# Kernel tuning notes

Hardware: AMD Instinct MI355X
Metric: run time of the kernel (lower is better)

Reference implementation:

```python
import jax, jax.numpy as jnp
import numpy as np
from jax import lax

ALPHA = 2.0
EROSIONS = 10


def setup_inputs() -> dict:
    key = jax.random.key(0)
    k1, k2 = jax.random.split(key)
    B, C, H, W = 32, 1, 1024, 1024
    pred = jax.random.uniform(k1, (B, C, H, W), dtype=jnp.float32)
    target = jax.random.uniform(k2, (B, C, H, W), dtype=jnp.float32)
    return {"pred": pred, "target": target}


def _hausdorff_er_loss(pred, target):
    # 3x3 cross structuring element * 0.2 (sums to 1), as in kernel2D
    kernel = jnp.array([[0.0, 0.2, 0.0],
                        [0.2, 0.2, 0.2],
                        [0.0, 0.2, 0.0]], dtype=pred.dtype)
    kernel = kernel[None, None]  # OIHW: (1,1,3,3)

    bound = (pred - target) ** 2  # (B,1,H,W)

    def step(carry, k):
        b, acc = carry
        # scipy.ndimage.convolve(mode='constant', cval=0) == SAME zero-padded conv;
        # the cross kernel is symmetric so correlation == convolution.
        dil = lax.conv_general_dilated(
            b, kernel, window_strides=(1, 1), padding='SAME',
            dimension_numbers=('NCHW', 'OIHW', 'NCHW'))
        er = jnp.maximum(dil - 0.5, 0.0)
        # per-sample min/max normalization (ptp over the whole (1,H,W) array)
        emin = er.min(axis=(1, 2, 3), keepdims=True)
        emax = er.max(axis=(1, 2, 3), keepdims=True)
        ptp = emax - emin
        er = jnp.where(ptp > 0, (er - emin) / jnp.where(ptp > 0, ptp, 1.0), er)
        acc = acc + er * (k + 1.0) ** ALPHA
        return (er, acc), None

    ks = jnp.arange(EROSIONS, dtype=bound.dtype)
    (_, eroted), _ = lax.scan(step, (bound, jnp.zeros_like(bound)), ks)
    return eroted.mean()


def reference(pred, target):
    return _hausdorff_er_loss(pred, target)
```

## Files before the change

### kernel.cpp

```cpp
#include <hip/hip_runtime.h>

#define BATCH 32
#define HH 1024
#define WW 1024
#define NPIX (HH * WW)
#define NEROS 10
#define TPS 64
#define NTILES (BATCH * TPS)
#define NB0 (BATCH * 128)
#define FRPS 1024

__device__ __forceinline__ float4 ld4f(const float* p) {
    return *reinterpret_cast<const float4*>(p);
}


__global__ __launch_bounds__(512, 8) void conv0_kernel(
    const float* __restrict__ pred, const float* __restrict__ tgt,
    float* __restrict__ out, unsigned short* __restrict__ Fout,
    unsigned* __restrict__ cntOut, unsigned* __restrict__ omin,
    unsigned* __restrict__ omax, double* __restrict__ osum) {
    int blk = blockIdx.x;
    blk = (blk & 7) * (NB0 >> 3) + (blk >> 3);
    const int s = blk >> 7, ty = blk & 127, ry = ty << 3;
    const int tid = threadIdx.x, lane = tid & 63, w = tid >> 6;
    const size_t sbase = (size_t)s * NPIX;

    __shared__ float sb[10 * 1024];

    float4 pv[5], tv[5];
#pragma unroll
    for (int i = 0; i < 5; ++i) {
        const int slot = tid + 512 * i;
        const int y = ry - 1 + (slot >> 8);
        if (y >= 0 && y < HH) {
            const size_t idx = sbase + (size_t)y * WW + ((slot & 255) << 2);
            pv[i] = ld4f(pred + idx);
            tv[i] = ld4f(tgt + idx);
        } else {
            pv[i] = make_float4(0.f, 0.f, 0.f, 0.f);
            tv[i] = make_float4(0.f, 0.f, 0.f, 0.f);
        }
    }
#pragma unroll
    for (int i = 0; i < 5; ++i) {
        const int slot = tid + 512 * i;
        float4 b;
        b.x = (pv[i].x - tv[i].x) * (pv[i].x - tv[i].x);
        b.y = (pv[i].y - tv[i].y) * (pv[i].y - tv[i].y);
        b.z = (pv[i].z - tv[i].z) * (pv[i].z - tv[i].z);
        b.w = (pv[i].w - tv[i].w) * (pv[i].w - tv[i].w);
        *reinterpret_cast<float4*>(
            &sb[(slot >> 8) * 1024 + ((slot & 255) << 2)]) = b;
    }
    __syncthreads();

    float lmin = 3.4e38f, lmax = 0.f, lsum = 0.f;
    unsigned rowmask = 0u;
    const int y = ry + w;
#pragma unroll
    for (int q = 0; q < 4; ++q) {
        const int xw = (q << 8) + (lane << 2);
        const float4 U = *(const float4*)&sb[w * 1024 + xw];
        const float4 Cc = *(const float4*)&sb[(w + 1) * 1024 + xw];
        const float4 D = *(const float4*)&sb[(w + 2) * 1024 + xw];
        float lf = __shfl_up(Cc.w, 1);
        if (lane == 0) lf = (q > 0) ? sb[(w + 1) * 1024 + (q << 8) - 1] : 0.f;
        float rt = __shfl_down(Cc.x, 1);
        if (lane == 63)
            rt = (q < 3) ? sb[(w + 1) * 1024 + (q << 8) + 256] : 0.f;
        const float cv[4] = {Cc.x, Cc.y, Cc.z, Cc.w};
        const float uv[4] = {U.x, U.y, U.z, U.w};
        const float dv[4] = {D.x, D.y, D.z, D.w};
        const float lvv[4] = {lf, Cc.x, Cc.y, Cc.z};
        const float rvv[4] = {Cc.y, Cc.z, Cc.w, rt};
        float O[4];
        bool nz = false;
#pragma unroll
        for (int j = 0; j < 4; ++j) {
            const float conv = 0.2f * (uv[j] + dv[j] + cv[j] + lvv[j] + rvv[j]);
            const float er = fmaxf(conv - 0.5f, 0.f);
            O[j] = er;
            lmin = fminf(lmin, er);
            lmax = fmaxf(lmax, er);
            lsum += er;
            nz = nz || (er > 0.f);
        }
        const unsigned long long bal = __ballot(nz);
        const bool myChunk =
            ((bal >> ((lane >> 4) << 4)) & 0xFFFFull) != 0ull;
        if (myChunk)
            *reinterpret_cast<float4*>(out + sbase + (size_t)y * WW + xw) =
                make_float4(O[0], O[1], O[2], O[3]);
        unsigned g = 0;
        if ((bal)&0xFFFFull) g |= 1u;
        if ((bal >> 16) & 0xFFFFull) g |= 2u;
        if ((bal >> 32) & 0xFFFFull) g |= 4u;
        if ((bal >> 48) & 0xFFFFull) g |= 8u;
        rowmask |= g << (q << 2);
    }
    if (lane == 0) Fout[s * FRPS + y] = (unsigned short)rowmask;

#pragma unroll
    for (int off = 32; off > 0; off >>= 1) {
        lmin = fminf(lmin, __shfl_down(lmin, off));
        lmax = fmaxf(lmax, __shfl_down(lmax, off));
        lsum += __shfl_down(lsum, off);
    }
    __shared__ float smn[8], smx[8], ssm[8];
    __shared__ unsigned sfb[8];
    if (lane == 0) {
        smn[w] = lmin;
        smx[w] = lmax;
        ssm[w] = lsum;
        sfb[w] = rowmask;
    }
    __syncthreads();
    if (tid == 0) {
        unsigned any = sfb[0];
        float bmn = smn[0], bmx = smx[0], bsm = ssm[0];
#pragma unroll
        for (int i = 1; i < 8; ++i) {
            bmn = fminf(bmn, smn[i]);
            bmx = fmaxf(bmx, smx[i]);
            bsm += ssm[i];
            any |= sfb[i];
        }
        if (any) atomicAdd(cntOut, 1u);
        atomicMin(&omin[s], __float_as_uint(bmn));
        if (bmx > 0.f) atomicMax(&omax[s], __float_as_uint(bmx));
        if (bsm > 0.f) atomicAdd(&osum[s], (double)bsm);
    }
}

__global__ __launch_bounds__(256, 4) void convt_kernel(
    const float* __restrict__ in, float* __restrict__ out,
    const unsigned short* __restrict__ Fprev, unsigned short* __restrict__ Fout,
    const unsigned* __restrict__ cntPrev, unsigned* __restrict__ cntOut,
    const unsigned* __restrict__ pmin, const unsigned* __restrict__ pmax,
    unsigned* __restrict__ omin, unsigned* __restrict__ omax,
    double* __restrict__ osum) {
    if (*cntPrev == 0u) return;

    int blk = blockIdx.x;
    blk = (blk & 7) * (NTILES >> 3) + (blk >> 3);
    const int s = blk >> 6, ty = blk & 63, ry = ty << 4;
    const int tid = threadIdx.x, lane = tid & 63, w = tid >> 6;
    const int xb = lane << 4;
    const size_t sbase = (size_t)s * NPIX;

    __shared__ unsigned short sM[18];
    __shared__ int sSkip;
    if (tid < 18) {
        const int yy = ry - 1 + tid;
        sM[tid] =
            (yy >= 0 && yy < HH) ? Fprev[s * FRPS + yy] : (unsigned short)0;
    }
    __syncthreads();
    if (tid == 0) {
        unsigned any = 0;
#pragma unroll
        for (int i = 0; i < 18; ++i) any |= sM[i];
        sSkip = (any == 0u);
    }
    __syncthreads();
    if (sSkip) {
        if (tid == 0) atomicMin(&omin[s], 0u);
        return;
    }

    float a = 1.f, cc = 0.f;
    {
        const float mn = __uint_as_float(pmin[s]);
        const float mx = __uint_as_float(pmax[s]);
        const float ptp = mx - mn;
        if (ptp > 0.f) { a = 1.f / ptp; cc = mn; }
    }

    const int r0 = w << 2;
    float A[16], B[16], C[16], O[16];

    auto loadRow = [&](int y, float* V) {
        const unsigned mask = sM[y - ry + 1];
        if (!((mask >> (lane >> 2)) & 1u)) {
#pragma unroll
            for (int j = 0; j < 16; ++j) V[j] = 0.f;
            return;
        }
        const size_t idx = sbase + (size_t)y * WW + xb;
#pragma unroll
        for (int q = 0; q < 4; ++q) {
            const float4 v = ld4f(in + idx + 4 * q);
            V[4 * q + 0] = v.x;
            V[4 * q + 1] = v.y;
            V[4 * q + 2] = v.z;
            V[4 * q + 3] = v.w;
        }
    };

    loadRow(ry + r0 - 1, A);
    loadRow(ry + r0, B);

    float lmin = 3.4e38f, lmax = 0.f, lsum = 0.f;
    unsigned blockAny = 0u;

#pragma unroll
    for (int r = 0; r < 4; ++r) {
        const int y = ry + r0 + r;
        loadRow(y + 1, C);
        const int mi = r0 + r + 1;
        const bool act = (sM[mi - 1] | sM[mi] | sM[mi + 1]) != 0;
        if (act) {
            float lfe = __shfl_up(B[15], 1);
            if (lane == 0) lfe = 0.f;
            float rte = __shfl_down(B[0], 1);
            if (lane == 63) rte = 0.f;
            const float vert =
                1.f + (y > 0 ? 1.f : 0.f) + (y < HH - 1 ? 1.f : 0.f);
            bool nz = false;
#pragma unroll
            for (int j = 0; j < 16; ++j) {
                const float lf = (j == 0) ? lfe : B[j - 1];
                const float rt = (j == 15) ? rte : B[j + 1];
                const float conv = 0.2f * (A[j] + C[j] + B[j] + lf + rt);
                const int x = xb + j;
                const float kf = 0.2f * (vert + (x > 0 ? 1.f : 0.f) +
                                         (x < WW - 1 ? 1.f : 0.f));
                const float dil = (conv - cc * kf) * a;
                const float er = fmaxf(dil - 0.5f, 0.f);
                O[j] = er;
                lmin = fminf(lmin, er);
                lmax = fmaxf(lmax, er);
                lsum += er;
                nz = nz || (er > 0.f);
            }
            const unsigned long long bal = __ballot(nz);
            if (((bal >> ((lane >> 2) << 2)) & 0xFull) != 0ull) {
                const size_t oidx = sbase + (size_t)y * WW + xb;
#pragma unroll
                for (int q = 0; q < 4; ++q)
                    *reinterpret_cast<float4*>(out + oidx + 4 * q) =
                        make_float4(O[4 * q], O[4 * q + 1], O[4 * q + 2],
                                    O[4 * q + 3]);
            }
            unsigned rm = 0;
#pragma unroll
            for (int c = 0; c < 16; ++c)
                if ((bal >> (c << 2)) & 0xFull) rm |= 1u << c;
            if (lane == 0) Fout[s * FRPS + y] = (unsigned short)rm;
            blockAny |= rm;
        } else {
            lmin = fminf(lmin, 0.f);
        }
#pragma unroll
        for (int j = 0; j < 16; ++j) {
            A[j] = B[j];
            B[j] = C[j];
        }
    }

#pragma unroll
    for (int off = 32; off > 0; off >>= 1) {
        lmin = fminf(lmin, __shfl_down(lmin, off));
        lmax = fmaxf(lmax, __shfl_down(lmax, off));
        lsum += __shfl_down(lsum, off);
    }
    __shared__ float smn[4], smx[4], ssm[4];
    __shared__ unsigned sfb[4];
    if (lane == 0) {
        smn[w] = lmin;
        smx[w] = lmax;
        ssm[w] = lsum;
        sfb[w] = blockAny;
    }
    __syncthreads();
    if (tid == 0) {
        const unsigned any = sfb[0] | sfb[1] | sfb[2] | sfb[3];
        float bmn = smn[0], bmx = smx[0], bsm = ssm[0];
#pragma unroll
        for (int i = 1; i < 4; ++i) {
            bmn = fminf(bmn, smn[i]);
            bmx = fmaxf(bmx, smx[i]);
            bsm += ssm[i];
        }
        if (any) atomicAdd(cntOut, 1u);
        atomicMin(&omin[s], __float_as_uint(bmn));
        if (bmx > 0.f) atomicMax(&omax[s], __float_as_uint(bmx));
        if (bsm > 0.f) atomicAdd(&osum[s], (double)bsm);
    }
}

__global__ void init_kernel(unsigned* __restrict__ minb,
                            unsigned* __restrict__ maxb,
                            double* __restrict__ sums,
                            unsigned* __restrict__ F16u,
                            unsigned* __restrict__ cnt) {
    const int i = blockIdx.x * blockDim.x + threadIdx.x;
    if (i < NEROS * BATCH) {
        minb[i] = 0x7f800000u;
        maxb[i] = 0u;
        sums[i] = 0.0;
    }
    if (i < NEROS * BATCH * FRPS / 2) F16u[i] = 0u;
    if (i < NEROS) cnt[i] = 0u;
}

__global__ void final_kernel(const unsigned* __restrict__ minb,
                             const unsigned* __restrict__ maxb,
                             const double* __restrict__ sums,
                             float* __restrict__ out) {
    const int s = threadIdx.x;
    double tot = 0.0;
    if (s < BATCH) {
        for (int k = 0; k < NEROS; ++k) {
            const float mn = __uint_as_float(minb[k * BATCH + s]);
            const float mx = __uint_as_float(maxb[k * BATCH + s]);
            const double sm = sums[k * BATCH + s];
            const float ptp = mx - mn;
            double v;
            if (ptp > 0.f)
                v = (sm - (double)NPIX * (double)mn) / (double)ptp;
            else
                v = sm;
            tot += (double)((k + 1) * (k + 1)) * v;
        }
    }
#pragma unroll
    for (int off = 32; off > 0; off >>= 1) tot += __shfl_down(tot, off);
    if (s == 0) out[0] = (float)(tot / ((double)BATCH * (double)NPIX));
}

extern "C" void kernel_launch(void* const* d_in, const int* in_sizes, int n_in,
                              void* d_out, int out_size, void* d_ws,
                              size_t ws_size, hipStream_t stream) {
    const float* pred = (const float*)d_in[0];
    const float* tgt = (const float*)d_in[1];
    float* out = (float*)d_out;

    float* buf0 = (float*)d_ws;
    float* buf1 = buf0 + (size_t)BATCH * NPIX;
    unsigned* minb = (unsigned*)(buf1 + (size_t)BATCH * NPIX);
    unsigned* maxb = minb + NEROS * BATCH;
    double* sums = (double*)(maxb + NEROS * BATCH);
    unsigned short* F = (unsigned short*)(sums + NEROS * BATCH);
    unsigned* cnt = (unsigned*)(F + (size_t)NEROS * BATCH * FRPS);

    init_kernel<<<640, 256, 0, stream>>>(minb, maxb, sums, (unsigned*)F, cnt);

    conv0_kernel<<<NB0, 512, 0, stream>>>(pred, tgt, buf0, F, &cnt[0], minb,
                                          maxb, sums);

    float* bufs[2] = {buf0, buf1};
    for (int k = 1; k < NEROS; ++k) {
        const float* src = bufs[(k - 1) & 1];
        float* dst = bufs[k & 1];
        convt_kernel<<<NTILES, 256, 0, stream>>>(
            src, dst, F + (size_t)(k - 1) * BATCH * FRPS,
            F + (size_t)k * BATCH * FRPS, &cnt[k - 1], &cnt[k],
            minb + (size_t)(k - 1) * BATCH, maxb + (size_t)(k - 1) * BATCH,
            minb + (size_t)k * BATCH, maxb + (size_t)k * BATCH,
            sums + (size_t)k * BATCH);
    }

    final_kernel<<<1, 64, 0, stream>>>(minb, maxb, sums, out);
}
```

Baseline: 122.5 us.

## Split conv0 tiles into half-width blocks with direct global-to-LDS loads

The first erosion kernel now handles half-width (512-column) tiles, doubling the block count. It loads raw pred and target rows straight into LDS with global_load_lds instead of staging through registers, and computes the squared difference on read. Halo columns at the half boundary come from scalar global loads, and the per-row flag mask is written as one byte per half. This aims to cut register pressure and improve load latency hiding, at the cost of twice the LDS reads and squared-difference work per pixel, plus extra halo loads.

```diff
diff --git a/kernel.cpp b/kernel.cpp
--- a/kernel.cpp
+++ b/kernel.cpp
@@ -7,7 +7,7 @@
 #define NEROS 10
 #define TPS 64
 #define NTILES (BATCH * TPS)
-#define NB0 (BATCH * 128)
+#define NB0 (BATCH * 256)
 #define FRPS 1024
 
 __device__ __forceinline__ float4 ld4f(const float* p) {
@@ -15,70 +15,119 @@
 }
 
 
-__global__ __launch_bounds__(512, 8) void conv0_kernel(
+__global__ __launch_bounds__(512, 6) void conv0_kernel(
     const float* __restrict__ pred, const float* __restrict__ tgt,
     float* __restrict__ out, unsigned short* __restrict__ Fout,
     unsigned* __restrict__ cntOut, unsigned* __restrict__ omin,
     unsigned* __restrict__ omax, double* __restrict__ osum) {
     int blk = blockIdx.x;
     blk = (blk & 7) * (NB0 >> 3) + (blk >> 3);
-    const int s = blk >> 7, ty = blk & 127, ry = ty << 3;
+    const int s = blk >> 8, rest = blk & 255;
+    const int ty = rest >> 1, half = rest & 1;
+    const int ry = ty << 3;
+    const int x0 = half << 9;
     const int tid = threadIdx.x, lane = tid & 63, w = tid >> 6;
     const size_t sbase = (size_t)s * NPIX;
 
-    __shared__ float sb[10 * 1024];
-
-    float4 pv[5], tv[5];
+    __shared__ float sb[20 * 512];
+    __shared__ float smn[8], smx[8], ssm[8];
+    __shared__ unsigned sfb[8];
+
 #pragma unroll
     for (int i = 0; i < 5; ++i) {
-        const int slot = tid + 512 * i;
-        const int y = ry - 1 + (slot >> 8);
+        const int sid = w * 5 + i;
+        const int slot = sid >> 1, seg = sid & 1;
+        const bool isP = slot < 10;
+        const int y = ry - 1 + (isP ? slot : slot - 10);
         if (y >= 0 && y < HH) {
-            const size_t idx = sbase + (size_t)y * WW + ((slot & 255) << 2);
-            pv[i] = ld4f(pred + idx);
-            tv[i] = ld4f(tgt + idx);
+            const float* g = (isP ? pred : tgt) + sbase + (size_t)y * WW + x0 +
+                             (seg << 8) + (lane << 2);
+            __builtin_amdgcn_global_load_lds(
+                (const __attribute__((address_space(1))) unsigned*)(const
+                                                                    void*)g,
+                (__attribute__((address_space(3))) unsigned*)(void*)&sb
+                    [(slot << 9) + (seg << 8)],
+                16, 0, 0);
         } else {
-            pv[i] = make_float4(0.f, 0.f, 0.f, 0.f);
-            tv[i] = make_float4(0.f, 0.f, 0.f, 0.f);
-        }
-    }
-#pragma unroll
-    for (int i = 0; i < 5; ++i) {
-        const int slot = tid + 512 * i;
-        float4 b;
-        b.x = (pv[i].x - tv[i].x) * (pv[i].x - tv[i].x);
-        b.y = (pv[i].y - tv[i].y) * (pv[i].y - tv[i].y);
-        b.z = (pv[i].z - tv[i].z) * (pv[i].z - tv[i].z);
-        b.w = (pv[i].w - tv[i].w) * (pv[i].w - tv[i].w);
-        *reinterpret_cast<float4*>(
-            &sb[(slot >> 8) * 1024 + ((slot & 255) << 2)]) = b;
+            *reinterpret_cast<float4*>(
+                &sb[(slot << 9) + (seg << 8) + (lane << 2)]) =
+                make_float4(0.f, 0.f, 0.f, 0.f);
+        }
+    }
+
+    const int y = ry + w;
+    float peL = 0.f, teL = 0.f, peR = 0.f, teR = 0.f;
+    if (lane == 0 && x0 > 0) {
+        const size_t g = sbase + (size_t)y * WW + x0 - 1;
+        peL = pred[g];
+        teL = tgt[g];
+    }
+    if (lane == 63 && x0 + 512 < WW) {
+        const size_t g = sbase + (size_t)y * WW + x0 + 512;
+        peR = pred[g];
+        teR = tgt[g];
     }
     __syncthreads();
 
+    const int pu = w, pc = w + 1, pd = w + 2;
+    const int tu = w + 10, tc = w + 11, td = w + 12;
     float lmin = 3.4e38f, lmax = 0.f, lsum = 0.f;
-    unsigned rowmask = 0u;
-    const int y = ry + w;
-#pragma unroll
-    for (int q = 0; q < 4; ++q) {
+    unsigned mask8 = 0u;
+
+#pragma unroll
+    for (int q = 0; q < 2; ++q) {
         const int xw = (q << 8) + (lane << 2);
-        const float4 U = *(const float4*)&sb[w * 1024 + xw];
-        const float4 Cc = *(const float4*)&sb[(w + 1) * 1024 + xw];
-        const float4 D = *(const float4*)&sb[(w + 2) * 1024 + xw];
-        float lf = __shfl_up(Cc.w, 1);
-        if (lane == 0) lf = (q > 0) ? sb[(w + 1) * 1024 + (q << 8) - 1] : 0.f;
-        float rt = __shfl_down(Cc.x, 1);
-        if (lane == 63)
-            rt = (q < 3) ? sb[(w + 1) * 1024 + (q << 8) + 256] : 0.f;
-        const float cv[4] = {Cc.x, Cc.y, Cc.z, Cc.w};
-        const float uv[4] = {U.x, U.y, U.z, U.w};
-        const float dv[4] = {D.x, D.y, D.z, D.w};
-        const float lvv[4] = {lf, Cc.x, Cc.y, Cc.z};
-        const float rvv[4] = {Cc.y, Cc.z, Cc.w, rt};
+        const float4 PU = *(const float4*)&sb[(pu << 9) + xw];
+        const float4 PC = *(const float4*)&sb[(pc << 9) + xw];
+        const float4 PD = *(const float4*)&sb[(pd << 9) + xw];
+        const float4 TU = *(const float4*)&sb[(tu << 9) + xw];
+        const float4 TC = *(const float4*)&sb[(tc << 9) + xw];
+        const float4 TD = *(const float4*)&sb[(td << 9) + xw];
+        float bU[4], bC[4], bD[4];
+        bU[0] = (PU.x - TU.x) * (PU.x - TU.x);
+        bU[1] = (PU.y - TU.y) * (PU.y - TU.y);
+        bU[2] = (PU.z - TU.z) * (PU.z - TU.z);
+        bU[3] = (PU.w - TU.w) * (PU.w - TU.w);
+        bC[0] = (PC.x - TC.x) * (PC.x - TC.x);
+        bC[1] = (PC.y - TC.y) * (PC.y - TC.y);
+        bC[2] = (PC.z - TC.z) * (PC.z - TC.z);
+        bC[3] = (PC.w - TC.w) * (PC.w - TC.w);
+        bD[0] = (PD.x - TD.x) * (PD.x - TD.x);
+        bD[1] = (PD.y - TD.y) * (PD.y - TD.y);
+        bD[2] = (PD.z - TD.z) * (PD.z - TD.z);
+        bD[3] = (PD.w - TD.w) * (PD.w - TD.w);
+
+        float lf = __shfl_up(bC[3], 1);
+        if (lane == 0) {
+            if (q == 1) {
+                const float pp = sb[(pc << 9) + 255];
+                const float tt = sb[(tc << 9) + 255];
+                lf = (pp - tt) * (pp - tt);
+            } else {
+                const float d = peL - teL;
+                lf = (x0 > 0) ? d * d : 0.f;
+            }
+        }
+        float rt = __shfl_down(bC[0], 1);
+        if (lane == 63) {
+            if (q == 0) {
+                const float pp = sb[(pc << 9) + 256];
+                const float tt = sb[(tc << 9) + 256];
+                rt = (pp - tt) * (pp - tt);
+            } else {
+                const float d = peR - teR;
+                rt = (x0 + 512 < WW) ? d * d : 0.f;
+            }
+        }
+        const float lv[4] = {lf, bC[0], bC[1], bC[2]};
+        const float rv[4] = {bC[1], bC[2], bC[3], rt};
+
         float O[4];
         bool nz = false;
 #pragma unroll
         for (int j = 0; j < 4; ++j) {
-            const float conv = 0.2f * (uv[j] + dv[j] + cv[j] + lvv[j] + rvv[j]);
+            const float conv =
+                0.2f * (bU[j] + bD[j] + bC[j] + lv[j] + rv[j]);
             const float er = fmaxf(conv - 0.5f, 0.f);
             O[j] = er;
             lmin = fminf(lmin, er);
@@ -87,19 +136,20 @@
             nz = nz || (er > 0.f);
         }
         const unsigned long long bal = __ballot(nz);
-        const bool myChunk =
-            ((bal >> ((lane >> 4) << 4)) & 0xFFFFull) != 0ull;
-        if (myChunk)
-            *reinterpret_cast<float4*>(out + sbase + (size_t)y * WW + xw) =
+        if ((bal >> ((lane >> 4) << 4)) & 0xFFFFull)
+            *reinterpret_cast<float4*>(out + sbase + (size_t)y * WW + x0 +
+                                       xw) =
                 make_float4(O[0], O[1], O[2], O[3]);
-        unsigned g = 0;
-        if ((bal)&0xFFFFull) g |= 1u;
-        if ((bal >> 16) & 0xFFFFull) g |= 2u;
-        if ((bal >> 32) & 0xFFFFull) g |= 4u;
-        if ((bal >> 48) & 0xFFFFull) g |= 8u;
-        rowmask |= g << (q << 2);
-    }
-    if (lane == 0) Fout[s * FRPS + y] = (unsigned short)rowmask;
+        unsigned nib = 0u;
+        if (bal & 0xFFFFull) nib |= 1u;
+        if ((bal >> 16) & 0xFFFFull) nib |= 2u;
+        if ((bal >> 32) & 0xFFFFull) nib |= 4u;
+        if ((bal >> 48) & 0xFFFFull) nib |= 8u;
+        mask8 |= nib << (q << 2);
+    }
+    if (lane == 0)
+        ((unsigned char*)Fout)[(((unsigned)(s << 10) + y) << 1) + half] =
+            (unsigned char)mask8;
 
 #pragma unroll
     for (int off = 32; off > 0; off >>= 1) {
@@ -107,13 +157,11 @@
         lmax = fmaxf(lmax, __shfl_down(lmax, off));
         lsum += __shfl_down(lsum, off);
     }
-    __shared__ float smn[8], smx[8], ssm[8];
-    __shared__ unsigned sfb[8];
     if (lane == 0) {
         smn[w] = lmin;
         smx[w] = lmax;
         ssm[w] = lsum;
-        sfb[w] = rowmask;
+        sfb[w] = mask8;
     }
     __syncthreads();
     if (tid == 0) {
```

Result: slower. 164.5 us (+34.3%).
